# Kernel tuning notes

Measured on AMD Instinct MI355X. Metric: run time of the kernel, lower is better.

Reference implementation:

```python
import jax, jax.numpy as jnp
import numpy as np

N_NODES = 50000


def gcn_conv(x, edge_index, W, b, n_nodes):
    # PyG GCNConv: h = D^{-1/2} (A + I) D^{-1/2} (x @ W) + b
    loops = jnp.arange(n_nodes, dtype=edge_index.dtype)
    src = jnp.concatenate([edge_index[0], loops])
    dst = jnp.concatenate([edge_index[1], loops])
    deg = jax.ops.segment_sum(jnp.ones_like(dst, dtype=x.dtype), dst,
                              num_segments=n_nodes)
    dinv = jnp.where(deg > 0, jax.lax.rsqrt(deg), 0.0)
    norm = dinv[src] * dinv[dst]                      # [E+N]
    h = x @ W                                          # [N, out]
    msg = h[src] * norm[:, None]                       # gather + scale
    out = jax.ops.segment_sum(msg, dst, num_segments=n_nodes)
    return out + b


def setup_inputs() -> dict:
    key = jax.random.key(0)
    ks = jax.random.split(key, 8)
    in_c, hid_c, out_c = 256, 128, 64
    x = jax.random.normal(ks[0], (N_NODES, in_c), dtype=jnp.float32)
    edge_index = jax.random.randint(ks[1], (2, 800000), 0, N_NODES, dtype=jnp.int64)
    pos_edge_index = jax.random.randint(ks[2], (2, 200000), 0, N_NODES, dtype=jnp.int64)
    neg_edge_index = jax.random.randint(ks[3], (2, 200000), 0, N_NES if False else N_NODES, dtype=jnp.int64)
    W1 = jax.random.normal(ks[4], (in_c, hid_c), dtype=jnp.float32) / np.sqrt(in_c)
    b1 = jnp.zeros((hid_c,), dtype=jnp.float32)
    W2 = jax.random.normal(ks[5], (hid_c, out_c), dtype=jnp.float32) / np.sqrt(hid_c)
    b2 = jnp.zeros((out_c,), dtype=jnp.float32)
    return {"x": x, "edge_index": edge_index, "pos_edge_index": pos_edge_index,
            "neg_edge_index": neg_edge_index, "W1": W1, "b1": b1, "W2": W2, "b2": b2}


def reference(x, edge_index, pos_edge_index, neg_edge_index, W1, b1, W2, b2):
    n = x.shape[0]
    h = jax.nn.relu(gcn_conv(x, edge_index, W1, b1, n))
    z = gcn_conv(h, edge_index, W2, b2, n)             # [N, out_c]
    ei = jnp.concatenate([pos_edge_index, neg_edge_index], axis=-1)
    logits = jnp.sum(z[ei[0]] * z[ei[1]], axis=-1)     # [E_pos + E_neg]
    return logits
```

## Files before the change

### kernel.cpp

```cpp
#include <hip/hip_runtime.h>
#include <stdint.h>

constexpr int N_NODES = 50000;
constexpr int E_EDGES = 800000;
constexpr int E_PAIR  = 200000;
constexpr int C_IN    = 256;
constexpr int C_HID   = 128;
constexpr int C_OUT   = 64;
constexpr int SLOT    = 64;

constexpr int NBUCK = 196;
constexpr int BCAP  = 4608;
constexpr int CHUNK = 2048;
constexpr int GEMM1_BLOCKS = (N_NODES + 63) / 64;

typedef __attribute__((ext_vector_type(8))) short bf8_t;
typedef __attribute__((ext_vector_type(8))) _Float16 f16x8;
typedef __attribute__((ext_vector_type(4))) float f32x4;

__device__ inline uint16_t f2bf(float f) {
    union { float f; uint32_t u; } c; c.f = f;
    uint32_t u = c.u + 0x7fff + ((c.u >> 16) & 1);
    return (uint16_t)(u >> 16);
}
__device__ inline uint32_t pack2bf(float a, float b) {
    union { float f; uint32_t u; } ca, cb; ca.f = a; cb.f = b;
    uint32_t ua = ca.u + 0x7fff + ((ca.u >> 16) & 1);
    uint32_t ub = cb.u + 0x7fff + ((cb.u >> 16) & 1);
    return (ua >> 16) | ((ub >> 16) << 16);
}
__device__ inline uint16_t f2h_bits(float v) {
    union { _Float16 h; uint16_t u; } c; c.h = (_Float16)v;
    return c.u;
}
__device__ inline uint32_t pack2h(float a, float b) {
    return (uint32_t)f2h_bits(a) | ((uint32_t)f2h_bits(b) << 16);
}
__device__ inline void acc_bf8(float* a, uint4 v) {
    const uint32_t p[4] = {v.x, v.y, v.z, v.w};
#pragma unroll
    for (int i = 0; i < 4; ++i) {
        union { uint32_t u; float f; } lo, hi;
        lo.u = p[i] << 16; hi.u = p[i] & 0xffff0000u;
        a[2 * i]     += lo.f;
        a[2 * i + 1] += hi.f;
    }
}
__device__ inline void acc_bf8s(float* a, uint4 v, float s) {
    const uint32_t p[4] = {v.x, v.y, v.z, v.w};
#pragma unroll
    for (int i = 0; i < 4; ++i) {
        union { uint32_t u; float f; } lo, hi;
        lo.u = p[i] << 16; hi.u = p[i] & 0xffff0000u;
        a[2 * i]     += lo.f * s;
        a[2 * i + 1] += hi.f * s;
    }
}
__device__ inline float dot_bf8(uint4 a, uint4 b) {
    const uint32_t pa[4] = {a.x, a.y, a.z, a.w};
    const uint32_t pb[4] = {b.x, b.y, b.z, b.w};
    float v = 0.f;
#pragma unroll
    for (int i = 0; i < 4; ++i) {
        union { uint32_t u; float f; } al, ah, bl, bh;
        al.u = pa[i] << 16; ah.u = pa[i] & 0xffff0000u;
        bl.u = pb[i] << 16; bh.u = pb[i] & 0xffff0000u;
        v += al.f * bl.f + ah.f * bh.f;
    }
    return v;
}

template<int N>
__device__ inline int wswz_idx(int k, int n) {
    int c = k >> 5, kq = (k >> 3) & 3, kk = k & 7, ct = n >> 4, nn = n & 15;
    return (((c * (N / 16) + ct) * 4 + kq) * 16 + nn) * 8 + kk;
}

__global__ __launch_bounds__(256) void prep_kernel(
        const float* __restrict__ W1, const float* __restrict__ W2,
        uint16_t* __restrict__ s1, uint16_t* __restrict__ s2,
        int* __restrict__ gcur) {
    int id = blockIdx.x * 256 + threadIdx.x;
    if (id < NBUCK) gcur[id] = 0;
    if (id < C_IN * C_HID) {
        int idx = wswz_idx<C_HID>(id / C_HID, id & (C_HID - 1));
        s1[idx] = f2h_bits(W1[id]);
    } else if (id < C_IN * C_HID + C_HID * C_OUT) {
        int id2 = id - C_IN * C_HID;
        int idx = wswz_idx<C_OUT>(id2 / C_OUT, id2 & (C_OUT - 1));
        s2[idx] = f2h_bits(W2[id2]);
    }
}

__global__ __launch_bounds__(256) void binA_kernel(
        const int* __restrict__ src, const int* __restrict__ dst,
        int* __restrict__ gcur, uint32_t* __restrict__ ebuf) {
    __shared__ int cnt[NBUCK], loc[NBUCK], lim[NBUCK], abase[NBUCK], wcur[NBUCK];
    __shared__ int tot;
    __shared__ uint32_t stag[CHUNK];
    __shared__ uint8_t  bof[CHUNK];

    const int t  = threadIdx.x;
    const int e0 = blockIdx.x * CHUNK;
    const int n  = min(CHUNK, E_EDGES - e0);

    for (int b = t; b < NBUCK; b += 256) cnt[b] = 0;
    if (t == 0) tot = 0;
    __syncthreads();

    uint32_t pk[CHUNK / 256]; int bk[CHUNK / 256];
    int ne = 0;
    for (int j = t; j < n; j += 256) {
        int d = dst[e0 + j], s = src[e0 + j];
        int b = d >> 8;
        pk[ne] = ((uint32_t)(d & 255) << 16) | (uint32_t)s;
        bk[ne] = b;
        atomicAdd(&cnt[b], 1);
        ++ne;
    }
    __syncthreads();
    for (int b = t; b < NBUCK; b += 256)
        loc[b] = atomicAdd(&tot, cnt[b]);
    __syncthreads();
    for (int b = t; b < NBUCK; b += 256) {
        int base = atomicAdd(&gcur[b], cnt[b]);
        int room = BCAP - base; if (room < 0) room = 0;
        lim[b]   = loc[b] + room;
        abase[b] = b * BCAP + base - loc[b];
        wcur[b]  = loc[b];
    }
    __syncthreads();
#pragma unroll
    for (int i = 0; i < CHUNK / 256; ++i) {
        if (i < ne) {
            int p = atomicAdd(&wcur[bk[i]], 1);
            stag[p] = pk[i];
            bof[p]  = (uint8_t)bk[i];
        }
    }
    __syncthreads();
    for (int j = t; j < n; j += 256) {
        int b = bof[j];
        if (j < lim[b]) ebuf[abase[b] + j] = stag[j];
    }
}

__global__ __launch_bounds__(256, 3) void build_gemm_kernel(
        const int* __restrict__ gcur, const uint32_t* __restrict__ ebuf,
        uint16_t* __restrict__ col2, int* __restrict__ degc,
        float* __restrict__ dinv,
        const float* __restrict__ A, const uint16_t* __restrict__ Bswz,
        uint16_t* __restrict__ out) {
    constexpr int K = C_IN, N = C_HID;
    constexpr int BM = 64, BK = 32;
    constexpr int CT   = N / 32;
    constexpr int NSUB = N / 16;
    constexpr int ABYTES = BM * BK * 2;
    constexpr int BBYTES = NSUB * 1024;
    __shared__ char sm[ABYTES + BBYTES];

    const int t = threadIdx.x;

    if (blockIdx.x < NBUCK) {
        int* cur = (int*)sm;
        const int b = blockIdx.x;
        cur[t] = 0;
        __syncthreads();

        int cn = gcur[b]; if (cn > BCAP) cn = BCAP;
        const uint32_t* eb = ebuf + (size_t)b * BCAP;
        const size_t nbase = (size_t)b << 8;

        int j = t;
        for (; j + 3 * 256 < cn; j += 4 * 256) {
            uint32_t v0 = eb[j], v1 = eb[j + 256], v2 = eb[j + 512], v3 = eb[j + 768];
            int p0 = atomicAdd(&cur[v0 >> 16], 1);
            int p1 = atomicAdd(&cur[v1 >> 16], 1);
            int p2 = atomicAdd(&cur[v2 >> 16], 1);
            int p3 = atomicAdd(&cur[v3 >> 16], 1);
            if (p0 < SLOT) col2[((nbase + (v0 >> 16)) << 6) + p0] = (uint16_t)(v0 & 0xffff);
            if (p1 < SLOT) col2[((nbase + (v1 >> 16)) << 6) + p1] = (uint16_t)(v1 & 0xffff);
            if (p2 < SLOT) col2[((nbase + (v2 >> 16)) << 6) + p2] = (uint16_t)(v2 & 0xffff);
            if (p3 < SLOT) col2[((nbase + (v3 >> 16)) << 6) + p3] = (uint16_t)(v3 & 0xffff);
        }
        for (; j < cn; j += 256) {
            uint32_t v = eb[j];
            int p = atomicAdd(&cur[v >> 16], 1);
            if (p < SLOT) col2[((nbase + (v >> 16)) << 6) + p] = (uint16_t)(v & 0xffff);
        }
        __syncthreads();
        int node = (int)nbase + t;
        if (node < N_NODES) {
            int dg = cur[t];
            degc[node] = dg;
            dinv[node] = rsqrtf((float)dg + 1.0f);
        }
        return;
    }

    char* As = sm;
    char* Bs = sm + ABYTES;

    const int lane = t & 63;
    const int w    = t >> 6;
    const int wrow = w & 1, wcol = w >> 1;
    const int m0   = (blockIdx.x - NBUCK) * BM;
    const int M    = N_NODES;

    const int sr = t >> 2, skq = t & 3;
    int arow = m0 + sr; if (arow > M - 1) arow = M - 1;
    const float* aptr = A + (size_t)arow * K + skq * 8;
    const int aslot = ((sr >> 4) * 64 + skq * 16 + (sr & 15)) * 16;

    f32x4 acc[2][CT];
#pragma unroll
    for (int rt = 0; rt < 2; ++rt)
#pragma unroll
        for (int ct = 0; ct < CT; ++ct) {
            f32x4 z = {0.f, 0.f, 0.f, 0.f};
            acc[rt][ct] = z;
        }

    const uint4* gh = (const uint4*)Bswz;

    constexpr int NCH = K / BK;
#pragma unroll 1
    for (int c = 0; c < NCH; ++c) {
        float4 v0 = *(const float4*)(aptr + c * BK);
        float4 v1 = *(const float4*)(aptr + c * BK + 4);
        uint4 bh0, bh1;
        {
            const uint4* ch = gh + (size_t)c * (BBYTES / 16);
            bh0 = ch[t];
            bh1 = ch[t + 256];
        }
        __syncthreads();
        {
            float e[8] = {v0.x, v0.y, v0.z, v0.w, v1.x, v1.y, v1.z, v1.w};
            uint32_t hp[4];
#pragma unroll
            for (int j = 0; j < 4; ++j)
                hp[j] = pack2h(e[2 * j], e[2 * j + 1]);
            *(uint4*)(As + aslot) = make_uint4(hp[0], hp[1], hp[2], hp[3]);
        }
        *(uint4*)(Bs + t * 16) = bh0;
        *(uint4*)(Bs + (t + 256) * 16) = bh1;
        __syncthreads();
        f16x8 Ah[2];
#pragma unroll
        for (int rt = 0; rt < 2; ++rt) {
            int st = wrow * 2 + rt;
            Ah[rt] = *(const f16x8*)(As + st * 1024 + lane * 16);
        }
#pragma unroll
        for (int ct = 0; ct < CT; ++ct) {
            int cg = wcol * CT + ct;
            f16x8 Bh = *(const f16x8*)(Bs + cg * 1024 + lane * 16);
#pragma unroll
            for (int rt = 0; rt < 2; ++rt)
                acc[rt][ct] = __builtin_amdgcn_mfma_f32_16x16x32_f16(Ah[rt], Bh, acc[rt][ct], 0, 0, 0);
        }
    }

#pragma unroll
    for (int rt = 0; rt < 2; ++rt) {
        int rowbase = m0 + wrow * 32 + rt * 16 + (lane >> 4) * 4;
#pragma unroll
        for (int ct = 0; ct < CT; ++ct) {
            int n = (wcol * CT + ct) * 16 + (lane & 15);
#pragma unroll
            for (int r = 0; r < 4; ++r) {
                int m = rowbase + r;
                if (m < M) out[(size_t)m * N + n] = f2bf(acc[rt][ct][r]);
            }
        }
    }
}

__global__ __launch_bounds__(256) void gather_gemm_kernel(
        const uint16_t* __restrict__ col2, const int* __restrict__ degc,
        const uint16_t* __restrict__ h0u, const float* __restrict__ dinv,
        const float* __restrict__ bias, const uint16_t* __restrict__ B2swz,
        uint16_t* __restrict__ z0s) {
    __shared__ uint4 hlds[256];
    const int t    = threadIdx.x;
    const int lane = t & 63;
    const int w    = t >> 6;
    const int sub  = lane >> 4;
    const int l    = lane & 15;
    const int node_loc = w * 4 + sub;
    const int node = blockIdx.x * 16 + node_loc;

    int dg = degc[node]; if (dg > SLOT) dg = SLOT;
    const float dn = dinv[node];
    const uint4* hs4 = (const uint4*)h0u;
    float a0[8], a1[8];
    {
        uint4 self = hs4[(size_t)node * 16 + l];
#pragma unroll
        for (int i = 0; i < 8; ++i) { a0[i] = 0.f; a1[i] = 0.f; }
        acc_bf8s(a0, self, dn);
    }
    const int base = node * SLOT;
    for (int c = 0; c * 16 < dg; ++c) {
        int cnt = dg - c * 16; if (cnt > 16) cnt = 16;
        int cv = (l < cnt) ? (int)col2[base + c * 16 + l] : 0;
        int j = 0;
        for (; j + 8 <= cnt; j += 8) {
            int s0 = __shfl(cv, sub * 16 + j,     64);
            int s1 = __shfl(cv, sub * 16 + j + 1, 64);
            int s2 = __shfl(cv, sub * 16 + j + 2, 64);
            int s3 = __shfl(cv, sub * 16 + j + 3, 64);
            int s4 = __shfl(cv, sub * 16 + j + 4, 64);
            int s5 = __shfl(cv, sub * 16 + j + 5, 64);
            int s6 = __shfl(cv, sub * 16 + j + 6, 64);
            int s7 = __shfl(cv, sub * 16 + j + 7, 64);
            uint4 v0 = hs4[(size_t)s0 * 16 + l];
            uint4 v1 = hs4[(size_t)s1 * 16 + l];
            uint4 v2 = hs4[(size_t)s2 * 16 + l];
            uint4 v3 = hs4[(size_t)s3 * 16 + l];
            uint4 v4 = hs4[(size_t)s4 * 16 + l];
            uint4 v5 = hs4[(size_t)s5 * 16 + l];
            uint4 v6 = hs4[(size_t)s6 * 16 + l];
            uint4 v7 = hs4[(size_t)s7 * 16 + l];
            float d0 = dinv[s0], d1 = dinv[s1], d2 = dinv[s2], d3 = dinv[s3];
            float d4 = dinv[s4], d5 = dinv[s5], d6 = dinv[s6], d7 = dinv[s7];
            acc_bf8s(a0, v0, d0); acc_bf8s(a1, v1, d1);
            acc_bf8s(a0, v2, d2); acc_bf8s(a1, v3, d3);
            acc_bf8s(a0, v4, d4); acc_bf8s(a1, v5, d5);
            acc_bf8s(a0, v6, d6); acc_bf8s(a1, v7, d7);
        }
        for (; j + 4 <= cnt; j += 4) {
            int s0 = __shfl(cv, sub * 16 + j,     64);
            int s1 = __shfl(cv, sub * 16 + j + 1, 64);
            int s2 = __shfl(cv, sub * 16 + j + 2, 64);
            int s3 = __shfl(cv, sub * 16 + j + 3, 64);
            uint4 v0 = hs4[(size_t)s0 * 16 + l];
            uint4 v1 = hs4[(size_t)s1 * 16 + l];
            uint4 v2 = hs4[(size_t)s2 * 16 + l];
            uint4 v3 = hs4[(size_t)s3 * 16 + l];
            float d0 = dinv[s0], d1 = dinv[s1], d2 = dinv[s2], d3 = dinv[s3];
            acc_bf8s(a0, v0, d0); acc_bf8s(a1, v1, d1);
            acc_bf8s(a0, v2, d2); acc_bf8s(a1, v3, d3);
        }
        for (; j < cnt; ++j) {
            int s = __shfl(cv, sub * 16 + j, 64);
            uint4 v = hs4[(size_t)s * 16 + l];
            acc_bf8s(a0, v, dinv[s]);
        }
    }
    {
        float4 bb0 = ((const float4*)bias)[2 * l];
        float4 bb1 = ((const float4*)bias)[2 * l + 1];
        float o[8];
        o[0] = fmaxf((a0[0] + a1[0]) * dn + bb0.x, 0.f);
        o[1] = fmaxf((a0[1] + a1[1]) * dn + bb0.y, 0.f);
        o[2] = fmaxf((a0[2] + a1[2]) * dn + bb0.z, 0.f);
        o[3] = fmaxf((a0[3] + a1[3]) * dn + bb0.w, 0.f);
        o[4] = fmaxf((a0[4] + a1[4]) * dn + bb1.x, 0.f);
        o[5] = fmaxf((a0[5] + a1[5]) * dn + bb1.y, 0.f);
        o[6] = fmaxf((a0[6] + a1[6]) * dn + bb1.z, 0.f);
        o[7] = fmaxf((a0[7] + a1[7]) * dn + bb1.w, 0.f);
        hlds[l * 16 + node_loc] = make_uint4(
            pack2h(o[0], o[1]), pack2h(o[2], o[3]),
            pack2h(o[4], o[5]), pack2h(o[6], o[7]));
    }
    __syncthreads();

    f32x4 acc = {0.f, 0.f, 0.f, 0.f};
    const char* hb = (const char*)hlds;
#pragma unroll
    for (int c = 0; c < 4; ++c) {
        f16x8 Af = *(const f16x8*)(hb + c * 1024 + lane * 16);
        f16x8 Bh = *(const f16x8*)(B2swz + (c * 4 + w) * 512 + lane * 8);
        acc = __builtin_amdgcn_mfma_f32_16x16x32_f16(Af, Bh, acc, 0, 0, 0);
    }
    const int colg = w * 16 + (lane & 15);
    const int rowb = blockIdx.x * 16 + (lane >> 4) * 4;
#pragma unroll
    for (int r = 0; r < 4; ++r) {
        int m = rowb + r;
        z0s[(size_t)m * C_OUT + colg] = f2bf(acc[r] * dinv[m]);
    }
}

template<int F, bool RELU>
__global__ __launch_bounds__(256) void gather_kernel(
        const uint16_t* __restrict__ col2, const int* __restrict__ degc,
        const uint16_t* __restrict__ hs, const float* __restrict__ dinv,
        const float* __restrict__ bias, uint16_t* __restrict__ out) {
    constexpr int LPN = F / 8;
    constexpr int NPW = 64 / LPN;
    const int lane = threadIdx.x & 63;
    const int sub  = lane / LPN;
    const int l    = lane % LPN;
    const int node = blockIdx.x * (4 * NPW) + (threadIdx.x >> 6) * NPW + sub;
    if (node >= N_NODES) return;

    int dg = degc[node]; if (dg > SLOT) dg = SLOT;
    const uint4* hs4 = (const uint4*)hs;

    float a0[8], a1[8];
    {
        uint4 self = hs4[(size_t)node * LPN + l];
#pragma unroll
        for (int i = 0; i < 8; ++i) { a0[i] = 0.f; a1[i] = 0.f; }
        acc_bf8(a0, self);
    }
    const int base = node * SLOT;

    for (int c = 0; c * LPN < dg; ++c) {
        int cnt = dg - c * LPN; if (cnt > LPN) cnt = LPN;
        int cv = (l < cnt) ? (int)col2[base + c * LPN + l] : 0;
        int j = 0;
        for (; j + 8 <= cnt; j += 8) {
            int s0 = __shfl(cv, sub * LPN + j,     64);
            int s1 = __shfl(cv, sub * LPN + j + 1, 64);
            int s2 = __shfl(cv, sub * LPN + j + 2, 64);
            int s3 = __shfl(cv, sub * LPN + j + 3, 64);
            int s4 = __shfl(cv, sub * LPN + j + 4, 64);
            int s5 = __shfl(cv, sub * LPN + j + 5, 64);
            int s6 = __shfl(cv, sub * LPN + j + 6, 64);
            int s7 = __shfl(cv, sub * LPN + j + 7, 64);
            uint4 v0 = hs4[(size_t)s0 * LPN + l];
            uint4 v1 = hs4[(size_t)s1 * LPN + l];
            uint4 v2 = hs4[(size_t)s2 * LPN + l];
            uint4 v3 = hs4[(size_t)s3 * LPN + l];
            uint4 v4 = hs4[(size_t)s4 * LPN + l];
            uint4 v5 = hs4[(size_t)s5 * LPN + l];
            uint4 v6 = hs4[(size_t)s6 * LPN + l];
            uint4 v7 = hs4[(size_t)s7 * LPN + l];
            acc_bf8(a0, v0); acc_bf8(a1, v1);
            acc_bf8(a0, v2); acc_bf8(a1, v3);
            acc_bf8(a0, v4); acc_bf8(a1, v5);
            acc_bf8(a0, v6); acc_bf8(a1, v7);
        }
        for (; j + 4 <= cnt; j += 4) {
            int s0 = __shfl(cv, sub * LPN + j,     64);
            int s1 = __shfl(cv, sub * LPN + j + 1, 64);
            int s2 = __shfl(cv, sub * LPN + j + 2, 64);
            int s3 = __shfl(cv, sub * LPN + j + 3, 64);
            uint4 v0 = hs4[(size_t)s0 * LPN + l];
            uint4 v1 = hs4[(size_t)s1 * LPN + l];
            uint4 v2 = hs4[(size_t)s2 * LPN + l];
            uint4 v3 = hs4[(size_t)s3 * LPN + l];
            acc_bf8(a0, v0); acc_bf8(a1, v1);
            acc_bf8(a0, v2); acc_bf8(a1, v3);
        }
        for (; j < cnt; ++j) {
            int s = __shfl(cv, sub * LPN + j, 64);
            uint4 v = hs4[(size_t)s * LPN + l];
            acc_bf8(a0, v);
        }
    }

    const float dn = dinv[node];
    float4 bb0 = ((const float4*)bias)[2 * l];
    float4 bb1 = ((const float4*)bias)[2 * l + 1];
    float o[8];
    o[0] = (a0[0] + a1[0]) * dn + bb0.x;
    o[1] = (a0[1] + a1[1]) * dn + bb0.y;
    o[2] = (a0[2] + a1[2]) * dn + bb0.z;
    o[3] = (a0[3] + a1[3]) * dn + bb0.w;
    o[4] = (a0[4] + a1[4]) * dn + bb1.x;
    o[5] = (a0[5] + a1[5]) * dn + bb1.y;
    o[6] = (a0[6] + a1[6]) * dn + bb1.z;
    o[7] = (a0[7] + a1[7]) * dn + bb1.w;
    if (RELU) {
#pragma unroll
        for (int i = 0; i < 8; ++i) o[i] = fmaxf(o[i], 0.f);
    }
    uint4 res = make_uint4(pack2bf(o[0], o[1]), pack2bf(o[2], o[3]),
                           pack2bf(o[4], o[5]), pack2bf(o[6], o[7]));
    ((uint4*)out)[(size_t)node * LPN + l] = res;
}

__global__ __launch_bounds__(256) void logits_kernel(
        const int* __restrict__ pos, const int* __restrict__ neg,
        const uint16_t* __restrict__ z, float* __restrict__ out) {
    const int t = threadIdx.x;
    const int l = t & 7;
    const int g = (blockIdx.x * 256 + t) >> 3;
    const int e0 = 2 * g;
    if (e0 >= 2 * E_PAIR) return;
    int s0, d0, s1, d1;
    if (e0 < E_PAIR) { s0 = pos[e0];          d0 = pos[E_PAIR + e0]; }
    else             { s0 = neg[e0 - E_PAIR]; d0 = neg[e0];          }
    int e1 = e0 + 1;
    if (e1 < E_PAIR) { s1 = pos[e1];          d1 = pos[E_PAIR + e1]; }
    else             { s1 = neg[e1 - E_PAIR]; d1 = neg[e1];          }
    const uint4* z4 = (const uint4*)z;
    uint4 ua0 = z4[(size_t)s0 * 8 + l];
    uint4 ub0 = z4[(size_t)d0 * 8 + l];
    uint4 ua1 = z4[(size_t)s1 * 8 + l];
    uint4 ub1 = z4[(size_t)d1 * 8 + l];
    float v0 = dot_bf8(ua0, ub0);
    float v1 = dot_bf8(ua1, ub1);
    v0 += __shfl_xor(v0, 1, 64); v1 += __shfl_xor(v1, 1, 64);
    v0 += __shfl_xor(v0, 2, 64); v1 += __shfl_xor(v1, 2, 64);
    v0 += __shfl_xor(v0, 4, 64); v1 += __shfl_xor(v1, 4, 64);
    if (l == 0) { out[e0] = v0; out[e1] = v1; }
}

extern "C" void kernel_launch(void* const* d_in, const int* in_sizes, int n_in,
                              void* d_out, int out_size, void* d_ws, size_t ws_size,
                              hipStream_t stream) {
    const float* x   = (const float*)d_in[0];
    const int*   ei  = (const int*)d_in[1];
    const int*   pos = (const int*)d_in[2];
    const int*   neg = (const int*)d_in[3];
    const float* W1  = (const float*)d_in[4];
    const float* b1  = (const float*)d_in[5];
    const float* W2  = (const float*)d_in[6];
    const float* b2  = (const float*)d_in[7];
    float* out = (float*)d_out;

    const int* src = ei;
    const int* dst = ei + E_EDGES;

    char* ws = (char*)d_ws;
    int*      degc  = (int*)ws;
    float*    dinv  = (float*)(ws + 200704);
    uint16_t* col2  = (uint16_t*)(ws + 401408);
    int*      gcur  = (int*)(ws + 6801408);
    uint16_t* B1swz = (uint16_t*)(ws + 6802432);
    uint16_t* B2swz = (uint16_t*)(ws + 6933504);
    uint16_t* h0u   = (uint16_t*)(ws + 6966272);
    uint16_t* z0s   = (uint16_t*)(ws + 32566272);
    uint16_t* zbuf  = (uint16_t*)(ws + 38966272);
    uint32_t* ebuf  = (uint32_t*)(ws + 45366272);

    prep_kernel<<<(C_IN * C_HID + C_HID * C_OUT + 255) / 256, 256, 0, stream>>>(
        W1, W2, B1swz, B2swz, gcur);

    binA_kernel<<<(E_EDGES + CHUNK - 1) / CHUNK, 256, 0, stream>>>(src, dst, gcur, ebuf);

    build_gemm_kernel<<<NBUCK + GEMM1_BLOCKS, 256, 0, stream>>>(
        gcur, ebuf, col2, degc, dinv, x, B1swz, h0u);

    gather_gemm_kernel<<<N_NODES / 16, 256, 0, stream>>>(
        col2, degc, h0u, dinv, b1, B2swz, z0s);

    gather_kernel<C_OUT, false><<<(N_NODES + 31) / 32, 256, 0, stream>>>(
        col2, degc, z0s, dinv, b2, zbuf);

    logits_kernel<<<(E_PAIR * 8 + 255) / 256, 256, 0, stream>>>(pos, neg, zbuf, out);
}
```

Baseline: 197.3 us.

## Replace two-pass bucketed CSR build with direct global-atomic slot insertion

Removes the binning kernel and the per-bucket shared-memory second pass. Each edge now does a global atomicAdd on its destination's degree counter and writes its source straight into that node's fixed slot array. The weight swizzle is fused into the same launch, and the degree counter is zeroed with a memset. This cuts one kernel launch and the ebuf round trip through memory. In exchange it relies on contended global atomics and scattered 2-byte writes, and the build blocks of the GEMM kernel now only compute dinv.

```diff
diff --git a/kernel.cpp b/kernel.cpp
--- a/kernel.cpp
+++ b/kernel.cpp
@@ -9,9 +9,9 @@
 constexpr int C_OUT   = 64;
 constexpr int SLOT    = 64;
 
-constexpr int NBUCK = 196;
-constexpr int BCAP  = 4608;
-constexpr int CHUNK = 2048;
+constexpr int PREPB  = 32;
+constexpr int BUILDB = (E_EDGES + 1023) / 1024;
+constexpr int NBUCK  = 196;
 constexpr int GEMM1_BLOCKS = (N_NODES + 63) / 64;
 
 typedef __attribute__((ext_vector_type(8))) short bf8_t;
@@ -76,79 +76,39 @@
     return (((c * (N / 16) + ct) * 4 + kq) * 16 + nn) * 8 + kk;
 }
 
-__global__ __launch_bounds__(256) void prep_kernel(
+__global__ __launch_bounds__(256) void prep_build_kernel(
         const float* __restrict__ W1, const float* __restrict__ W2,
         uint16_t* __restrict__ s1, uint16_t* __restrict__ s2,
-        int* __restrict__ gcur) {
-    int id = blockIdx.x * 256 + threadIdx.x;
-    if (id < NBUCK) gcur[id] = 0;
-    if (id < C_IN * C_HID) {
-        int idx = wswz_idx<C_HID>(id / C_HID, id & (C_HID - 1));
-        s1[idx] = f2h_bits(W1[id]);
-    } else if (id < C_IN * C_HID + C_HID * C_OUT) {
-        int id2 = id - C_IN * C_HID;
-        int idx = wswz_idx<C_OUT>(id2 / C_OUT, id2 & (C_OUT - 1));
-        s2[idx] = f2h_bits(W2[id2]);
-    }
-}
-
-__global__ __launch_bounds__(256) void binA_kernel(
         const int* __restrict__ src, const int* __restrict__ dst,
-        int* __restrict__ gcur, uint32_t* __restrict__ ebuf) {
-    __shared__ int cnt[NBUCK], loc[NBUCK], lim[NBUCK], abase[NBUCK], wcur[NBUCK];
-    __shared__ int tot;
-    __shared__ uint32_t stag[CHUNK];
-    __shared__ uint8_t  bof[CHUNK];
-
-    const int t  = threadIdx.x;
-    const int e0 = blockIdx.x * CHUNK;
-    const int n  = min(CHUNK, E_EDGES - e0);
-
-    for (int b = t; b < NBUCK; b += 256) cnt[b] = 0;
-    if (t == 0) tot = 0;
-    __syncthreads();
-
-    uint32_t pk[CHUNK / 256]; int bk[CHUNK / 256];
-    int ne = 0;
-    for (int j = t; j < n; j += 256) {
-        int d = dst[e0 + j], s = src[e0 + j];
-        int b = d >> 8;
-        pk[ne] = ((uint32_t)(d & 255) << 16) | (uint32_t)s;
-        bk[ne] = b;
-        atomicAdd(&cnt[b], 1);
-        ++ne;
-    }
-    __syncthreads();
-    for (int b = t; b < NBUCK; b += 256)
-        loc[b] = atomicAdd(&tot, cnt[b]);
-    __syncthreads();
-    for (int b = t; b < NBUCK; b += 256) {
-        int base = atomicAdd(&gcur[b], cnt[b]);
-        int room = BCAP - base; if (room < 0) room = 0;
-        lim[b]   = loc[b] + room;
-        abase[b] = b * BCAP + base - loc[b];
-        wcur[b]  = loc[b];
-    }
-    __syncthreads();
-#pragma unroll
-    for (int i = 0; i < CHUNK / 256; ++i) {
-        if (i < ne) {
-            int p = atomicAdd(&wcur[bk[i]], 1);
-            stag[p] = pk[i];
-            bof[p]  = (uint8_t)bk[i];
-        }
-    }
-    __syncthreads();
-    for (int j = t; j < n; j += 256) {
-        int b = bof[j];
-        if (j < lim[b]) ebuf[abase[b] + j] = stag[j];
+        int* __restrict__ degc, uint16_t* __restrict__ col2) {
+    if (blockIdx.x < PREPB) {
+        for (int id = blockIdx.x * 256 + threadIdx.x;
+             id < C_IN * C_HID + C_HID * C_OUT; id += PREPB * 256) {
+            if (id < C_IN * C_HID) {
+                int idx = wswz_idx<C_HID>(id / C_HID, id & (C_HID - 1));
+                s1[idx] = f2h_bits(W1[id]);
+            } else {
+                int id2 = id - C_IN * C_HID;
+                int idx = wswz_idx<C_OUT>(id2 / C_OUT, id2 & (C_OUT - 1));
+                s2[idx] = f2h_bits(W2[id2]);
+            }
+        }
+        return;
+    }
+    int e = (blockIdx.x - PREPB) * 1024 + threadIdx.x;
+#pragma unroll
+    for (int i = 0; i < 4; ++i, e += 256) {
+        if (e < E_EDGES) {
+            int d = dst[e];
+            int s = src[e];
+            int p = atomicAdd(&degc[d], 1);
+            if (p < SLOT) col2[((size_t)d << 6) + p] = (uint16_t)s;
+        }
     }
 }
 
 __global__ __launch_bounds__(256, 3) void build_gemm_kernel(
-        const int* __restrict__ gcur, const uint32_t* __restrict__ ebuf,
-        uint16_t* __restrict__ col2, int* __restrict__ degc,
-        float* __restrict__ dinv,
+        const int* __restrict__ degc, float* __restrict__ dinv,
         const float* __restrict__ A, const uint16_t* __restrict__ Bswz,
         uint16_t* __restrict__ out) {
     constexpr int K = C_IN, N = C_HID;
@@ -162,39 +122,9 @@
     const int t = threadIdx.x;
 
     if (blockIdx.x < NBUCK) {
-        int* cur = (int*)sm;
-        const int b = blockIdx.x;
-        cur[t] = 0;
-        __syncthreads();
-
-        int cn = gcur[b]; if (cn > BCAP) cn = BCAP;
-        const uint32_t* eb = ebuf + (size_t)b * BCAP;
-        const size_t nbase = (size_t)b << 8;
-
-        int j = t;
-        for (; j + 3 * 256 < cn; j += 4 * 256) {
-            uint32_t v0 = eb[j], v1 = eb[j + 256], v2 = eb[j + 512], v3 = eb[j + 768];
-            int p0 = atomicAdd(&cur[v0 >> 16], 1);
-            int p1 = atomicAdd(&cur[v1 >> 16], 1);
-            int p2 = atomicAdd(&cur[v2 >> 16], 1);
-            int p3 = atomicAdd(&cur[v3 >> 16], 1);
-            if (p0 < SLOT) col2[((nbase + (v0 >> 16)) << 6) + p0] = (uint16_t)(v0 & 0xffff);
-            if (p1 < SLOT) col2[((nbase + (v1 >> 16)) << 6) + p1] = (uint16_t)(v1 & 0xffff);
-            if (p2 < SLOT) col2[((nbase + (v2 >> 16)) << 6) + p2] = (uint16_t)(v2 & 0xffff);
-            if (p3 < SLOT) col2[((nbase + (v3 >> 16)) << 6) + p3] = (uint16_t)(v3 & 0xffff);
-        }
-        for (; j < cn; j += 256) {
-            uint32_t v = eb[j];
-            int p = atomicAdd(&cur[v >> 16], 1);
-            if (p < SLOT) col2[((nbase + (v >> 16)) << 6) + p] = (uint16_t)(v & 0xffff);
-        }
-        __syncthreads();
-        int node = (int)nbase + t;
-        if (node < N_NODES) {
-            int dg = cur[t];
-            degc[node] = dg;
-            dinv[node] = rsqrtf((float)dg + 1.0f);
-        }
+        int node = blockIdx.x * 256 + t;
+        if (node < N_NODES)
+            dinv[node] = rsqrtf((float)degc[node] + 1.0f);
         return;
     }
 
@@ -522,21 +452,19 @@
     int*      degc  = (int*)ws;
     float*    dinv  = (float*)(ws + 200704);
     uint16_t* col2  = (uint16_t*)(ws + 401408);
-    int*      gcur  = (int*)(ws + 6801408);
     uint16_t* B1swz = (uint16_t*)(ws + 6802432);
     uint16_t* B2swz = (uint16_t*)(ws + 6933504);
     uint16_t* h0u   = (uint16_t*)(ws + 6966272);
     uint16_t* z0s   = (uint16_t*)(ws + 32566272);
     uint16_t* zbuf  = (uint16_t*)(ws + 38966272);
-    uint32_t* ebuf  = (uint32_t*)(ws + 45366272);
-
-    prep_kernel<<<(C_IN * C_HID + C_HID * C_OUT + 255) / 256, 256, 0, stream>>>(
-        W1, W2, B1swz, B2swz, gcur);
-
-    binA_kernel<<<(E_EDGES + CHUNK - 1) / CHUNK, 256, 0, stream>>>(src, dst, gcur, ebuf);
+
+    hipMemsetAsync(degc, 0, N_NODES * sizeof(int), stream);
+
+    prep_build_kernel<<<PREPB + BUILDB, 256, 0, stream>>>(
+        W1, W2, B1swz, B2swz, src, dst, degc, col2);
 
     build_gemm_kernel<<<NBUCK + GEMM1_BLOCKS, 256, 0, stream>>>(
-        gcur, ebuf, col2, degc, dinv, x, B1swz, h0u);
+        degc, dinv, x, B1swz, h0u);
 
     gather_gemm_kernel<<<N_NODES / 16, 256, 0, stream>>>(
         col2, degc, h0u, dinv, b1, B2swz, z0s);
```

Measured after the change: 232.9 us. 1.18x slower.

## Split neighbor gathers across two teams per node and fuse prep into binning

Applied to the files above, without the earlier changes.

The two gather kernels now give each node twice as many lanes: two teams each take alternating 16- or 8-neighbor chunks, and the partial sums are combined with a cross-lane xor shuffle. This aims to expose more memory-level parallelism for the latency-bound random row gathers. The gather_gemm block grows to 512 threads, and only the first 256 threads run the MFMA epilogue. Separately, the weight-swizzle prep kernel is merged into the binning kernel as extra blocks, and the bucket-counter zeroing moves to a memset, removing one kernel launch. The trade-offs are extra shuffle work, half-idle lanes on low-degree nodes, and idle threads during the GEMM stage.

```diff
diff --git a/kernel.cpp b/kernel.cpp
--- a/kernel.cpp
+++ b/kernel.cpp
@@ -12,6 +12,8 @@
 constexpr int NBUCK = 196;
 constexpr int BCAP  = 4608;
 constexpr int CHUNK = 2048;
+constexpr int PREPB = 32;
+constexpr int BINAB = (E_EDGES + CHUNK - 1) / CHUNK;
 constexpr int GEMM1_BLOCKS = (N_NODES + 63) / 64;
 
 typedef __attribute__((ext_vector_type(8))) short bf8_t;
@@ -76,23 +78,9 @@
     return (((c * (N / 16) + ct) * 4 + kq) * 16 + nn) * 8 + kk;
 }
 
-__global__ __launch_bounds__(256) void prep_kernel(
+__global__ __launch_bounds__(256) void prep_binA_kernel(
         const float* __restrict__ W1, const float* __restrict__ W2,
         uint16_t* __restrict__ s1, uint16_t* __restrict__ s2,
-        int* __restrict__ gcur) {
-    int id = blockIdx.x * 256 + threadIdx.x;
-    if (id < NBUCK) gcur[id] = 0;
-    if (id < C_IN * C_HID) {
-        int idx = wswz_idx<C_HID>(id / C_HID, id & (C_HID - 1));
-        s1[idx] = f2h_bits(W1[id]);
-    } else if (id < C_IN * C_HID + C_HID * C_OUT) {
-        int id2 = id - C_IN * C_HID;
-        int idx = wswz_idx<C_OUT>(id2 / C_OUT, id2 & (C_OUT - 1));
-        s2[idx] = f2h_bits(W2[id2]);
-    }
-}
-
-__global__ __launch_bounds__(256) void binA_kernel(
         const int* __restrict__ src, const int* __restrict__ dst,
         int* __restrict__ gcur, uint32_t* __restrict__ ebuf) {
     __shared__ int cnt[NBUCK], loc[NBUCK], lim[NBUCK], abase[NBUCK], wcur[NBUCK];
@@ -100,8 +88,24 @@
     __shared__ uint32_t stag[CHUNK];
     __shared__ uint8_t  bof[CHUNK];
 
-    const int t  = threadIdx.x;
-    const int e0 = blockIdx.x * CHUNK;
+    const int t = threadIdx.x;
+
+    if (blockIdx.x < PREPB) {
+        for (int id = blockIdx.x * 256 + t;
+             id < C_IN * C_HID + C_HID * C_OUT; id += PREPB * 256) {
+            if (id < C_IN * C_HID) {
+                int idx = wswz_idx<C_HID>(id / C_HID, id & (C_HID - 1));
+                s1[idx] = f2h_bits(W1[id]);
+            } else {
+                int id2 = id - C_IN * C_HID;
+                int idx = wswz_idx<C_OUT>(id2 / C_OUT, id2 & (C_OUT - 1));
+                s2[idx] = f2h_bits(W2[id2]);
+            }
+        }
+        return;
+    }
+
+    const int e0 = (blockIdx.x - PREPB) * CHUNK;
     const int n  = min(CHUNK, E_EDGES - e0);
 
     for (int b = t; b < NBUCK; b += 256) cnt[b] = 0;
@@ -277,7 +281,7 @@
     }
 }
 
-__global__ __launch_bounds__(256) void gather_gemm_kernel(
+__global__ __launch_bounds__(512) void gather_gemm_kernel(
         const uint16_t* __restrict__ col2, const int* __restrict__ degc,
         const uint16_t* __restrict__ h0u, const float* __restrict__ dinv,
         const float* __restrict__ bias, const uint16_t* __restrict__ B2swz,
@@ -286,35 +290,40 @@
     const int t    = threadIdx.x;
     const int lane = t & 63;
     const int w    = t >> 6;
-    const int sub  = lane >> 4;
-    const int l    = lane & 15;
-    const int node_loc = w * 4 + sub;
+    const int g32  = lane >> 5;
+    const int q    = lane & 31;
+    const int team = q >> 4;
+    const int l    = q & 15;
+    const int node_loc = w * 2 + g32;
     const int node = blockIdx.x * 16 + node_loc;
 
     int dg = degc[node]; if (dg > SLOT) dg = SLOT;
     const float dn = dinv[node];
     const uint4* hs4 = (const uint4*)h0u;
     float a0[8], a1[8];
-    {
+#pragma unroll
+    for (int i = 0; i < 8; ++i) { a0[i] = 0.f; a1[i] = 0.f; }
+    if (team == 0) {
         uint4 self = hs4[(size_t)node * 16 + l];
-#pragma unroll
-        for (int i = 0; i < 8; ++i) { a0[i] = 0.f; a1[i] = 0.f; }
         acc_bf8s(a0, self, dn);
     }
     const int base = node * SLOT;
-    for (int c = 0; c * 16 < dg; ++c) {
-        int cnt = dg - c * 16; if (cnt > 16) cnt = 16;
-        int cv = (l < cnt) ? (int)col2[base + c * 16 + l] : 0;
+    const int wb   = (lane & 32) | (team << 4);
+
+    for (int c = 0; c * 32 < dg; ++c) {
+        int off = c * 32 + (team << 4);
+        int cnt = dg - off; if (cnt < 0) cnt = 0; if (cnt > 16) cnt = 16;
+        int cv = (l < cnt) ? (int)col2[base + off + l] : 0;
         int j = 0;
         for (; j + 8 <= cnt; j += 8) {
-            int s0 = __shfl(cv, sub * 16 + j,     64);
-            int s1 = __shfl(cv, sub * 16 + j + 1, 64);
-            int s2 = __shfl(cv, sub * 16 + j + 2, 64);
-            int s3 = __shfl(cv, sub * 16 + j + 3, 64);
-            int s4 = __shfl(cv, sub * 16 + j + 4, 64);
-            int s5 = __shfl(cv, sub * 16 + j + 5, 64);
-            int s6 = __shfl(cv, sub * 16 + j + 6, 64);
-            int s7 = __shfl(cv, sub * 16 + j + 7, 64);
+            int s0 = __shfl(cv, wb + j,     64);
+            int s1 = __shfl(cv, wb + j + 1, 64);
+            int s2 = __shfl(cv, wb + j + 2, 64);
+            int s3 = __shfl(cv, wb + j + 3, 64);
+            int s4 = __shfl(cv, wb + j + 4, 64);
+            int s5 = __shfl(cv, wb + j + 5, 64);
+            int s6 = __shfl(cv, wb + j + 6, 64);
+            int s7 = __shfl(cv, wb + j + 7, 64);
             uint4 v0 = hs4[(size_t)s0 * 16 + l];
             uint4 v1 = hs4[(size_t)s1 * 16 + l];
             uint4 v2 = hs4[(size_t)s2 * 16 + l];
@@ -331,10 +340,10 @@
             acc_bf8s(a0, v6, d6); acc_bf8s(a1, v7, d7);
         }
         for (; j + 4 <= cnt; j += 4) {
-            int s0 = __shfl(cv, sub * 16 + j,     64);
-            int s1 = __shfl(cv, sub * 16 + j + 1, 64);
-            int s2 = __shfl(cv, sub * 16 + j + 2, 64);
-            int s3 = __shfl(cv, sub * 16 + j + 3, 64);
+            int s0 = __shfl(cv, wb + j,     64);
+            int s1 = __shfl(cv, wb + j + 1, 64);
+            int s2 = __shfl(cv, wb + j + 2, 64);
+            int s3 = __shfl(cv, wb + j + 3, 64);
             uint4 v0 = hs4[(size_t)s0 * 16 + l];
             uint4 v1 = hs4[(size_t)s1 * 16 + l];
             uint4 v2 = hs4[(size_t)s2 * 16 + l];
@@ -344,43 +353,52 @@
             acc_bf8s(a0, v2, d2); acc_bf8s(a1, v3, d3);
         }
         for (; j < cnt; ++j) {
-            int s = __shfl(cv, sub * 16 + j, 64);
+            int s = __shfl(cv, wb + j, 64);
             uint4 v = hs4[(size_t)s * 16 + l];
             acc_bf8s(a0, v, dinv[s]);
         }
     }
     {
+        float av[8];
+#pragma unroll
+        for (int i = 0; i < 8; ++i) {
+            av[i] = a0[i] + a1[i];
+            av[i] += __shfl_xor(av[i], 16, 64);
+        }
         float4 bb0 = ((const float4*)bias)[2 * l];
         float4 bb1 = ((const float4*)bias)[2 * l + 1];
         float o[8];
-        o[0] = fmaxf((a0[0] + a1[0]) * dn + bb0.x, 0.f);
-        o[1] = fmaxf((a0[1] + a1[1]) * dn + bb0.y, 0.f);
-        o[2] = fmaxf((a0[2] + a1[2]) * dn + bb0.z, 0.f);
-        o[3] = fmaxf((a0[3] + a1[3]) * dn + bb0.w, 0.f);
-        o[4] = fmaxf((a0[4] + a1[4]) * dn + bb1.x, 0.f);
-        o[5] = fmaxf((a0[5] + a1[5]) * dn + bb1.y, 0.f);
-        o[6] = fmaxf((a0[6] + a1[6]) * dn + bb1.z, 0.f);
-        o[7] = fmaxf((a0[7] + a1[7]) * dn + bb1.w, 0.f);
-        hlds[l * 16 + node_loc] = make_uint4(
-            pack2h(o[0], o[1]), pack2h(o[2], o[3]),
-            pack2h(o[4], o[5]), pack2h(o[6], o[7]));
+        o[0] = fmaxf(av[0] * dn + bb0.x, 0.f);
+        o[1] = fmaxf(av[1] * dn + bb0.y, 0.f);
+        o[2] = fmaxf(av[2] * dn + bb0.z, 0.f);
+        o[3] = fmaxf(av[3] * dn + bb0.w, 0.f);
+        o[4] = fmaxf(av[4] * dn + bb1.x, 0.f);
+        o[5] = fmaxf(av[5] * dn + bb1.y, 0.f);
+        o[6] = fmaxf(av[6] * dn + bb1.z, 0.f);
+        o[7] = fmaxf(av[7] * dn + bb1.w, 0.f);
+        if (team == 0)
+            hlds[l * 16 + node_loc] = make_uint4(
+                pack2h(o[0], o[1]), pack2h(o[2], o[3]),
+                pack2h(o[4], o[5]), pack2h(o[6], o[7]));
     }
     __syncthreads();
 
-    f32x4 acc = {0.f, 0.f, 0.f, 0.f};
-    const char* hb = (const char*)hlds;
-#pragma unroll
-    for (int c = 0; c < 4; ++c) {
-        f16x8 Af = *(const f16x8*)(hb + c * 1024 + lane * 16);
-        f16x8 Bh = *(const f16x8*)(B2swz + (c * 4 + w) * 512 + lane * 8);
-        acc = __builtin_amdgcn_mfma_f32_16x16x32_f16(Af, Bh, acc, 0, 0, 0);
-    }
-    const int colg = w * 16 + (lane & 15);
-    const int rowb = blockIdx.x * 16 + (lane >> 4) * 4;
-#pragma unroll
-    for (int r = 0; r < 4; ++r) {
-        int m = rowb + r;
-        z0s[(size_t)m * C_OUT + colg] = f2bf(acc[r] * dinv[m]);
+    if (t < 256) {
+        f32x4 acc = {0.f, 0.f, 0.f, 0.f};
+        const char* hb = (const char*)hlds;
+#pragma unroll
+        for (int c = 0; c < 4; ++c) {
+            f16x8 Af = *(const f16x8*)(hb + c * 1024 + lane * 16);
+            f16x8 Bh = *(const f16x8*)(B2swz + (c * 4 + w) * 512 + lane * 8);
+            acc = __builtin_amdgcn_mfma_f32_16x16x32_f16(Af, Bh, acc, 0, 0, 0);
+        }
+        const int colg = w * 16 + (lane & 15);
+        const int rowb = blockIdx.x * 16 + (lane >> 4) * 4;
+#pragma unroll
+        for (int r = 0; r < 4; ++r) {
+            int m = rowb + r;
+            z0s[(size_t)m * C_OUT + colg] = f2bf(acc[r] * dinv[m]);
+        }
     }
 }
 
@@ -390,38 +408,40 @@
         const uint16_t* __restrict__ hs, const float* __restrict__ dinv,
         const float* __restrict__ bias, uint16_t* __restrict__ out) {
     constexpr int LPN = F / 8;
-    constexpr int NPW = 64 / LPN;
     const int lane = threadIdx.x & 63;
-    const int sub  = lane / LPN;
-    const int l    = lane % LPN;
-    const int node = blockIdx.x * (4 * NPW) + (threadIdx.x >> 6) * NPW + sub;
+    const int q    = lane & 15;
+    const int team = q >> 3;
+    const int l    = q & 7;
+    const int node = blockIdx.x * 16 + (threadIdx.x >> 6) * 4 + (lane >> 4);
     if (node >= N_NODES) return;
 
     int dg = degc[node]; if (dg > SLOT) dg = SLOT;
     const uint4* hs4 = (const uint4*)hs;
 
     float a0[8], a1[8];
-    {
+#pragma unroll
+    for (int i = 0; i < 8; ++i) { a0[i] = 0.f; a1[i] = 0.f; }
+    if (team == 0) {
         uint4 self = hs4[(size_t)node * LPN + l];
-#pragma unroll
-        for (int i = 0; i < 8; ++i) { a0[i] = 0.f; a1[i] = 0.f; }
         acc_bf8(a0, self);
     }
     const int base = node * SLOT;
-
-    for (int c = 0; c * LPN < dg; ++c) {
-        int cnt = dg - c * LPN; if (cnt > LPN) cnt = LPN;
-        int cv = (l < cnt) ? (int)col2[base + c * LPN + l] : 0;
+    const int wb   = (lane & 48) | (team << 3);
+
+    for (int c = 0; c * 16 < dg; ++c) {
+        int off = c * 16 + (team << 3);
+        int cnt = dg - off; if (cnt < 0) cnt = 0; if (cnt > 8) cnt = 8;
+        int cv = (l < cnt) ? (int)col2[base + off + l] : 0;
         int j = 0;
         for (; j + 8 <= cnt; j += 8) {
-            int s0 = __shfl(cv, sub * LPN + j,     64);
-            int s1 = __shfl(cv, sub * LPN + j + 1, 64);
-            int s2 = __shfl(cv, sub * LPN + j + 2, 64);
-            int s3 = __shfl(cv, sub * LPN + j + 3, 64);
-            int s4 = __shfl(cv, sub * LPN + j + 4, 64);
-            int s5 = __shfl(cv, sub * LPN + j + 5, 64);
-            int s6 = __shfl(cv, sub * LPN + j + 6, 64);
-            int s7 = __shfl(cv, sub * LPN + j + 7, 64);
+            int s0 = __shfl(cv, wb + j,     64);
+            int s1 = __shfl(cv, wb + j + 1, 64);
+            int s2 = __shfl(cv, wb + j + 2, 64);
+            int s3 = __shfl(cv, wb + j + 3, 64);
+            int s4 = __shfl(cv, wb + j + 4, 64);
+            int s5 = __shfl(cv, wb + j + 5, 64);
+            int s6 = __shfl(cv, wb + j + 6, 64);
+            int s7 = __shfl(cv, wb + j + 7, 64);
             uint4 v0 = hs4[(size_t)s0 * LPN + l];
             uint4 v1 = hs4[(size_t)s1 * LPN + l];
             uint4 v2 = hs4[(size_t)s2 * LPN + l];
@@ -436,10 +456,10 @@
             acc_bf8(a0, v6); acc_bf8(a1, v7);
         }
         for (; j + 4 <= cnt; j += 4) {
-            int s0 = __shfl(cv, sub * LPN + j,     64);
-            int s1 = __shfl(cv, sub * LPN + j + 1, 64);
-            int s2 = __shfl(cv, sub * LPN + j + 2, 64);
-            int s3 = __shfl(cv, sub * LPN + j + 3, 64);
+            int s0 = __shfl(cv, wb + j,     64);
+            int s1 = __shfl(cv, wb + j + 1, 64);
+            int s2 = __shfl(cv, wb + j + 2, 64);
+            int s3 = __shfl(cv, wb + j + 3, 64);
             uint4 v0 = hs4[(size_t)s0 * LPN + l];
             uint4 v1 = hs4[(size_t)s1 * LPN + l];
             uint4 v2 = hs4[(size_t)s2 * LPN + l];
@@ -448,31 +468,39 @@
             acc_bf8(a0, v2); acc_bf8(a1, v3);
         }
         for (; j < cnt; ++j) {
-            int s = __shfl(cv, sub * LPN + j, 64);
+            int s = __shfl(cv, wb + j, 64);
             uint4 v = hs4[(size_t)s * LPN + l];
             acc_bf8(a0, v);
         }
     }
 
     const float dn = dinv[node];
+    float av[8];
+#pragma unroll
+    for (int i = 0; i < 8; ++i) {
+        av[i] = a0[i] + a1[i];
+        av[i] += __shfl_xor(av[i], 8, 64);
+    }
     float4 bb0 = ((const float4*)bias)[2 * l];
     float4 bb1 = ((const float4*)bias)[2 * l + 1];
     float o[8];
-    o[0] = (a0[0] + a1[0]) * dn + bb0.x;
-    o[1] = (a0[1] + a1[1]) * dn + bb0.y;
-    o[2] = (a0[2] + a1[2]) * dn + bb0.z;
-    o[3] = (a0[3] + a1[3]) * dn + bb0.w;
-    o[4] = (a0[4] + a1[4]) * dn + bb1.x;
-    o[5] = (a0[5] + a1[5]) * dn + bb1.y;
-    o[6] = (a0[6] + a1[6]) * dn + bb1.z;
-    o[7] = (a0[7] + a1[7]) * dn + bb1.w;
+    o[0] = av[0] * dn + bb0.x;
+    o[1] = av[1] * dn + bb0.y;
+    o[2] = av[2] * dn + bb0.z;
+    o[3] = av[3] * dn + bb0.w;
+    o[4] = av[4] * dn + bb1.x;
+    o[5] = av[5] * dn + bb1.y;
+    o[6] = av[6] * dn + bb1.z;
+    o[7] = av[7] * dn + bb1.w;
     if (RELU) {
 #pragma unroll
         for (int i = 0; i < 8; ++i) o[i] = fmaxf(o[i], 0.f);
     }
-    uint4 res = make_uint4(pack2bf(o[0], o[1]), pack2bf(o[2], o[3]),
-                           pack2bf(o[4], o[5]), pack2bf(o[6], o[7]));
-    ((uint4*)out)[(size_t)node * LPN + l] = res;
+    if (team == 0) {
+        uint4 res = make_uint4(pack2bf(o[0], o[1]), pack2bf(o[2], o[3]),
+                               pack2bf(o[4], o[5]), pack2bf(o[6], o[7]));
+        ((uint4*)out)[(size_t)node * LPN + l] = res;
+    }
 }
 
 __global__ __launch_bounds__(256) void logits_kernel(
@@ -530,18 +558,18 @@
     uint16_t* zbuf  = (uint16_t*)(ws + 38966272);
     uint32_t* ebuf  = (uint32_t*)(ws + 45366272);
 
-    prep_kernel<<<(C_IN * C_HID + C_HID * C_OUT + 255) / 256, 256, 0, stream>>>(
-        W1, W2, B1swz, B2swz, gcur);
-
-    binA_kernel<<<(E_EDGES + CHUNK - 1) / CHUNK, 256, 0, stream>>>(src, dst, gcur, ebuf);
+    hipMemsetAsync(gcur, 0, NBUCK * sizeof(int), stream);
+
+    prep_binA_kernel<<<PREPB + BINAB, 256, 0, stream>>>(
+        W1, W2, B1swz, B2swz, src, dst, gcur, ebuf);
 
     build_gemm_kernel<<<NBUCK + GEMM1_BLOCKS, 256, 0, stream>>>(
         gcur, ebuf, col2, degc, dinv, x, B1swz, h0u);
 
-    gather_gemm_kernel<<<N_NODES / 16, 256, 0, stream>>>(
+    gather_gemm_kernel<<<N_NODES / 16, 512, 0, stream>>>(
         col2, degc, h0u, dinv, b1, B2swz, z0s);
 
-    gather_kernel<C_OUT, false><<<(N_NODES + 31) / 32, 256, 0, stream>>>(
+    gather_kernel<C_OUT, false><<<(N_NODES + 15) / 16, 256, 0, stream>>>(
         col2, degc, z0s, dinv, b2, zbuf);
 
     logits_kernel<<<(E_PAIR * 8 + 255) / 256, 256, 0, stream>>>(pos, neg, zbuf, out);
```

Result: slower. 209.8 us (+6.3%).
